# Performance work log

Hardware: AMD Instinct MI355X
Metric: run time of the kernel (lower is better)

## Reference

```python
import jax, jax.numpy as jnp
import numpy as np

# LIF constants from __init__ defaults and forward body
TAU = 20.0        # membrane time constant
TH = 1.0          # base threshold
TAU_ADAPT = 100.0 # adaptation time constant
BETA_ADAPT = 1.5  # adaptation strength
V_RESET = -0.5    # reset potential
K = 10.0          # surrogate sigmoid slope


def setup_inputs() -> dict:
    key = jax.random.key(0)
    I = jax.random.normal(key, (16384, 2048), dtype=jnp.float32)
    return {"I": I}


def reference(I):
    # I: (B, L). Sequential LIF recurrence over L via lax.scan.
    B, L = I.shape
    dtype = I.dtype

    def step(carry, I_t):
        v, a, s_num = carry  # each (B,)
        th_eff = TH + BETA_ADAPT * a
        v = v - v / TAU + I_t  # v += dv
        s_soft = jax.nn.sigmoid(K * (v - th_eff))
        s_hard = (v >= th_eff).astype(dtype)
        # straight-through: forward value = s_hard, grad flows via s_soft
        s = jax.lax.stop_gradient(s_hard - s_soft) + s_soft
        s_num = s_num + s
        s_det = jax.lax.stop_gradient(s)  # reset is non-differentiable (detached)
        v = v * (1.0 - s_det) + V_RESET * s_det
        a = a - a / TAU_ADAPT + s
        return (v, a, s_num), (s, s_num)

    zeros = jnp.zeros((B,), dtype)
    _, (spikes_t, series_t) = jax.lax.scan(step, (zeros, zeros, zeros), I.T)
    # scan outputs are (L, B); transpose back to (B, L)
    return spikes_t.T, series_t.T
```

## Files before the change

### kernel.cpp

```cpp
#include <hip/hip_runtime.h>


#define LIF_L  2048
#define TILE   64
#define NTILES (LIF_L / TILE)
#define STRIDE 65

__device__ __forceinline__ float div20(float v) {
    const float rh = 0.05f;
    float q0 = __fmul_rn(v, rh);
    float r  = __fmaf_rn(-20.0f, q0, v);
    return __fmaf_rn(r, rh, q0);
}

__device__ __forceinline__ float div100(float a) {
    const float rh = 0.01f;
    float q0 = __fmul_rn(a, rh);
    float r  = __fmaf_rn(-100.0f, q0, a);
    return __fmaf_rn(r, rh, q0);
}

__device__ __forceinline__ float lif_step(float It, float& v, float& a, float& snum) {
    float th = __fadd_rn(1.0f, __fmul_rn(1.5f, a));
    float vn = __fadd_rn(__fsub_rn(v, div20(v)), It);
    bool fire = (vn >= th);
    float s = fire ? 1.0f : 0.0f;
    snum = __fadd_rn(snum, s);
    v = fire ? -0.5f : vn;
    a = __fadd_rn(__fsub_rn(a, div100(a)), s);
    return s;
}

__global__ __launch_bounds__(64, 1) void lif_fwd(const float* __restrict__ I,
                                                 float* __restrict__ spikes,
                                                 float* __restrict__ series) {
    __shared__ float sp_tile[64 * STRIDE];
    __shared__ float se_tile[64 * STRIDE];

    const int lane = threadIdx.x;
    const int row0 = blockIdx.x * 64;
    const size_t rbase = (size_t)(row0 + lane) * LIF_L;
    const float4* __restrict__ I4 = reinterpret_cast<const float4*>(I + rbase);

    float v = 0.0f, a = 0.0f, snum = 0.0f;

    float4 bufA[16], bufB[16];

    #pragma unroll
    for (int i = 0; i < 16; ++i) bufA[i] = I4[i];
    #pragma unroll
    for (int i = 0; i < 16; ++i) bufB[i] = I4[16 + i];

    auto compute_tile = [&](float4* buf) {
        #pragma unroll
        for (int c = 0; c < 16; ++c) {
            float4 in = buf[c];
            float s0 = lif_step(in.x, v, a, snum); float n0 = snum;
            float s1 = lif_step(in.y, v, a, snum); float n1 = snum;
            float s2 = lif_step(in.z, v, a, snum); float n2 = snum;
            float s3 = lif_step(in.w, v, a, snum); float n3 = snum;
            int b = lane * STRIDE + c * 4;
            sp_tile[b + 0] = s0; sp_tile[b + 1] = s1;
            sp_tile[b + 2] = s2; sp_tile[b + 3] = s3;
            se_tile[b + 0] = n0; se_tile[b + 1] = n1;
            se_tile[b + 2] = n2; se_tile[b + 3] = n3;
        }
    };

    auto flush_tile = [&](int kt) {
        const size_t colbase = (size_t)kt * TILE;
        #pragma unroll
        for (int i = 0; i < 16; ++i) {
            int idx = i * 64 + lane;
            int row = idx >> 4;
            int c4  = (idx & 15) * 4;
            int lb  = row * STRIDE + c4;
            float4 vs = make_float4(sp_tile[lb], sp_tile[lb + 1],
                                    sp_tile[lb + 2], sp_tile[lb + 3]);
            float4 ve = make_float4(se_tile[lb], se_tile[lb + 1],
                                    se_tile[lb + 2], se_tile[lb + 3]);
            size_t g = (size_t)(row0 + row) * LIF_L + colbase + c4;
            *reinterpret_cast<float4*>(spikes + g) = vs;
            *reinterpret_cast<float4*>(series + g) = ve;
        }
    };

    for (int kt = 0; kt < NTILES; kt += 2) {
        compute_tile(bufA);
        if (kt + 2 < NTILES) {
            #pragma unroll
            for (int i = 0; i < 16; ++i) bufA[i] = I4[(kt + 2) * 16 + i];
        }
        flush_tile(kt);

        compute_tile(bufB);
        if (kt + 3 < NTILES) {
            #pragma unroll
            for (int i = 0; i < 16; ++i) bufB[i] = I4[(kt + 3) * 16 + i];
        }
        flush_tile(kt + 1);
    }
}

extern "C" void kernel_launch(void* const* d_in, const int* in_sizes, int n_in,
                              void* d_out, int out_size, void* d_ws, size_t ws_size,
                              hipStream_t stream) {
    const float* I = (const float*)d_in[0];
    const int B = in_sizes[0] / LIF_L;
    float* spikes = (float*)d_out;
    float* series = (float*)d_out + (size_t)B * LIF_L;

    const int threads = 64;
    const int blocks = B / threads;
    lif_fwd<<<blocks, threads, 0, stream>>>(I, spikes, series);
}
```

Measured before the change: 410.6 us.

## Specialize waves: one runs LIF recurrence, other does prefix sum and stores

Launches two waves per block: wave 0 runs the serial LIF recurrence and writes spikes into a double-buffered LDS tile. Wave 1 computes the running spike count and performs the coalesced global stores of both outputs for the previous tile. This takes the store and prefix-sum work off the latency-critical serial chain, at the cost of block-wide barriers each half-iteration and extra LDS.

```diff
diff --git a/kernel.cpp b/kernel.cpp
--- a/kernel.cpp
+++ b/kernel.cpp
@@ -20,63 +20,77 @@
     return __fmaf_rn(r, rh, q0);
 }
 
-__device__ __forceinline__ float lif_step(float It, float& v, float& a, float& snum) {
+__device__ __forceinline__ float lif_step(float It, float& v, float& a) {
     float th = __fadd_rn(1.0f, __fmul_rn(1.5f, a));
     float vn = __fadd_rn(__fsub_rn(v, div20(v)), It);
     bool fire = (vn >= th);
     float s = fire ? 1.0f : 0.0f;
-    snum = __fadd_rn(snum, s);
     v = fire ? -0.5f : vn;
     a = __fadd_rn(__fsub_rn(a, div100(a)), s);
     return s;
 }
 
-__global__ __launch_bounds__(64, 1) void lif_fwd(const float* __restrict__ I,
-                                                 float* __restrict__ spikes,
-                                                 float* __restrict__ series) {
-    __shared__ float sp_tile[64 * STRIDE];
+__global__ __launch_bounds__(128, 1) void lif_fwd(const float* __restrict__ I,
+                                                  float* __restrict__ spikes,
+                                                  float* __restrict__ series) {
+    __shared__ float sp_tile[2][64 * STRIDE];
     __shared__ float se_tile[64 * STRIDE];
 
-    const int lane = threadIdx.x;
+    const int tid  = threadIdx.x;
+    const int wave = tid >> 6;
+    const int lane = tid & 63;
     const int row0 = blockIdx.x * 64;
-    const size_t rbase = (size_t)(row0 + lane) * LIF_L;
-    const float4* __restrict__ I4 = reinterpret_cast<const float4*>(I + rbase);
 
-    float v = 0.0f, a = 0.0f, snum = 0.0f;
-
+    const float4* __restrict__ I4 =
+        reinterpret_cast<const float4*>(I + (size_t)(row0 + lane) * LIF_L);
+    float v = 0.0f, a = 0.0f;
     float4 bufA[16], bufB[16];
 
-    #pragma unroll
-    for (int i = 0; i < 16; ++i) bufA[i] = I4[i];
-    #pragma unroll
-    for (int i = 0; i < 16; ++i) bufB[i] = I4[16 + i];
+    float carry = 0.0f;
 
-    auto compute_tile = [&](float4* buf) {
+    if (wave == 0) {
+        #pragma unroll
+        for (int i = 0; i < 16; ++i) bufA[i] = I4[i];
+        #pragma unroll
+        for (int i = 0; i < 16; ++i) bufB[i] = I4[16 + i];
+    }
+
+    auto compute_tile = [&](const float4* buf, float* sp) {
         #pragma unroll
         for (int c = 0; c < 16; ++c) {
             float4 in = buf[c];
-            float s0 = lif_step(in.x, v, a, snum); float n0 = snum;
-            float s1 = lif_step(in.y, v, a, snum); float n1 = snum;
-            float s2 = lif_step(in.z, v, a, snum); float n2 = snum;
-            float s3 = lif_step(in.w, v, a, snum); float n3 = snum;
+            float s0 = lif_step(in.x, v, a);
+            float s1 = lif_step(in.y, v, a);
+            float s2 = lif_step(in.z, v, a);
+            float s3 = lif_step(in.w, v, a);
             int b = lane * STRIDE + c * 4;
-            sp_tile[b + 0] = s0; sp_tile[b + 1] = s1;
-            sp_tile[b + 2] = s2; sp_tile[b + 3] = s3;
-            se_tile[b + 0] = n0; se_tile[b + 1] = n1;
-            se_tile[b + 2] = n2; se_tile[b + 3] = n3;
+            sp[b + 0] = s0; sp[b + 1] = s1;
+            sp[b + 2] = s2; sp[b + 3] = s3;
         }
     };
 
-    auto flush_tile = [&](int kt) {
-        const size_t colbase = (size_t)kt * TILE;
+    auto helper_tile = [&](int tkt, const float* sp) {
+        const int rb = lane * STRIDE;
+        #pragma unroll
+        for (int c = 0; c < 16; ++c) {
+            float4 sv = make_float4(sp[rb + c*4], sp[rb + c*4 + 1],
+                                    sp[rb + c*4 + 2], sp[rb + c*4 + 3]);
+            float4 nv;
+            carry = __fadd_rn(carry, sv.x); nv.x = carry;
+            carry = __fadd_rn(carry, sv.y); nv.y = carry;
+            carry = __fadd_rn(carry, sv.z); nv.z = carry;
+            carry = __fadd_rn(carry, sv.w); nv.w = carry;
+            se_tile[rb + c*4 + 0] = nv.x; se_tile[rb + c*4 + 1] = nv.y;
+            se_tile[rb + c*4 + 2] = nv.z; se_tile[rb + c*4 + 3] = nv.w;
+        }
+        const size_t colbase = (size_t)tkt * TILE;
         #pragma unroll
         for (int i = 0; i < 16; ++i) {
             int idx = i * 64 + lane;
             int row = idx >> 4;
             int c4  = (idx & 15) * 4;
             int lb  = row * STRIDE + c4;
-            float4 vs = make_float4(sp_tile[lb], sp_tile[lb + 1],
-                                    sp_tile[lb + 2], sp_tile[lb + 3]);
+            float4 vs = make_float4(sp[lb], sp[lb + 1], sp[lb + 2], sp[lb + 3]);
             float4 ve = make_float4(se_tile[lb], se_tile[lb + 1],
                                     se_tile[lb + 2], se_tile[lb + 3]);
             size_t g = (size_t)(row0 + row) * LIF_L + colbase + c4;
@@ -86,20 +100,28 @@
     };
 
     for (int kt = 0; kt < NTILES; kt += 2) {
-        compute_tile(bufA);
-        if (kt + 2 < NTILES) {
-            #pragma unroll
-            for (int i = 0; i < 16; ++i) bufA[i] = I4[(kt + 2) * 16 + i];
+        if (wave == 0) {
+            compute_tile(bufA, sp_tile[0]);
+            if (kt + 2 < NTILES) {
+                #pragma unroll
+                for (int i = 0; i < 16; ++i) bufA[i] = I4[(kt + 2) * 16 + i];
+            }
+        } else if (kt > 0) {
+            helper_tile(kt - 1, sp_tile[1]);
         }
-        flush_tile(kt);
-
-        compute_tile(bufB);
-        if (kt + 3 < NTILES) {
-            #pragma unroll
-            for (int i = 0; i < 16; ++i) bufB[i] = I4[(kt + 3) * 16 + i];
+        __syncthreads();
+        if (wave == 0) {
+            compute_tile(bufB, sp_tile[1]);
+            if (kt + 3 < NTILES) {
+                #pragma unroll
+                for (int i = 0; i < 16; ++i) bufB[i] = I4[(kt + 3) * 16 + i];
+            }
+        } else {
+            helper_tile(kt, sp_tile[0]);
         }
-        flush_tile(kt + 1);
+        __syncthreads();
     }
+    if (wave == 1) helper_tile(NTILES - 1, sp_tile[1]);
 }
 
 extern "C" void kernel_launch(void* const* d_in, const int* in_sizes, int n_in,
@@ -110,7 +132,7 @@
     float* spikes = (float*)d_out;
     float* series = (float*)d_out + (size_t)B * LIF_L;
 
-    const int threads = 64;
-    const int blocks = B / threads;
+    const int threads = 128;
+    const int blocks = B / 64;
     lif_fwd<<<blocks, threads, 0, stream>>>(I, spikes, series);
 }
```

Result: faster. 390.4 us (-4.9%).
